# Optimization experiments

Hardware: AMD Instinct MI355X
Metric: run time of the kernel (lower is better)

Reference implementation:

```python
import jax, jax.numpy as jnp
import numpy as np

N = 1_000_000
VOCAB = 50_000
EMBED_DIM = 128
ENCODE_DIM = 128


def _random_preorder_tree(n, seed=0):
    """Generate a random tree whose nodes are numbered in pre-order DFS.
    Returns subtree_end[i] = index of the last node in node i's subtree (inclusive)."""
    rng = np.random.default_rng(seed)
    parent = np.empty(n, dtype=np.int64)
    parent[0] = -1
    stack = [0]
    pops = rng.geometric(0.5, size=n) - 1  # how far up to climb before attaching
    for i in range(1, n):
        npop = min(int(pops[i]), len(stack) - 1)
        for _ in range(npop):
            stack.pop()
        parent[i] = stack[-1]
        stack.append(i)
    end = np.arange(n, dtype=np.int64)
    for i in range(n - 1, 0, -1):
        p = parent[i]
        if end[p] < end[i]:
            end[p] = end[i]
    return end


def setup_inputs() -> dict:
    key = jax.random.key(0)
    k1, k2, k3, k4 = jax.random.split(key, 4)
    tokens = jax.random.randint(k1, (N,), 0, VOCAB, dtype=jnp.int64).astype(jnp.int32)
    subtree_end = jnp.asarray(_random_preorder_tree(N), dtype=jnp.int32)
    embedding_weight = jax.random.normal(k2, (VOCAB, EMBED_DIM), dtype=jnp.float32)
    W = jax.random.normal(k3, (ENCODE_DIM, EMBED_DIM), dtype=jnp.float32) * (1.0 / np.sqrt(EMBED_DIM))
    b = jax.random.normal(k4, (ENCODE_DIM,), dtype=jnp.float32) * 0.01
    return {"tokens": tokens, "subtree_end": subtree_end,
            "embedding_weight": embedding_weight, "W": W, "b": b}


def reference(tokens, subtree_end, embedding_weight, W, b):
    # Per-node contribution: x_i = Linear(Embed(token_i))          [N, encode_dim]
    x = embedding_weight[tokens] @ W.T + b
    # h_i = sum of x over subtree(i). With pre-order DFS numbering, the subtree
    # of i is the contiguous range [i, subtree_end[i]], so use an inclusive
    # prefix sum: h_i = S[end_i] - S[i] + x_i.
    S = jnp.cumsum(x, axis=0)                                      # [N, encode_dim]
    h = S[subtree_end] - S + x                                     # [N, encode_dim]
    # pool = max over all node hidden states (order-independent)
    return jnp.max(h, axis=0)                                      # [encode_dim]
```

## Files before the change

### kernel.cpp

```cpp
#include <hip/hip_runtime.h>
#include <hip/hip_bf16.h>

#define D      128
#define LG     9
#define CHUNK  512

typedef __attribute__((ext_vector_type(8))) short          short8;
typedef __attribute__((ext_vector_type(8))) unsigned short ushort8;
typedef __attribute__((ext_vector_type(4))) float          floatx4;
typedef __attribute__((ext_vector_type(2))) float          floatx2;

__device__ inline float b2f(unsigned short u) {
    return __uint_as_float(((unsigned)u) << 16);
}
__device__ inline unsigned short f2bf(float f) {
    __hip_bfloat16 h = __float2bfloat16(f);
    unsigned short u;
    __builtin_memcpy(&u, &h, 2);
    return u;
}
__device__ inline short8 u2s(ushort8 u) {
    short8 s; __builtin_memcpy(&s, &u, 16); return s;
}
__device__ inline void atomicMaxF(float* addr, float v) {
    if (v >= 0.f) atomicMax((int*)addr, __float_as_int(v));
    else          atomicMin((unsigned int*)addr, __float_as_uint(v));
}

__global__ void init_out_kernel(float* out, int out_size) {
    int t = threadIdx.x;
    if (t < out_size) out[t] = -INFINITY;
}

__global__ __launch_bounds__(256) void chunk_sums_kernel(
        const int* __restrict__ tokens, const float* __restrict__ emb,
        float* __restrict__ sumE, int n, int C) {
    __shared__ int toks[4][CHUNK];
    int tid = threadIdx.x, w = tid >> 6, lane = tid & 63;
    int cb = min(blockIdx.x * 4 + w, C - 1);
    int i0 = cb << LG, cnt = min(CHUNK, n - i0);
    for (int t = lane; t < cnt; t += 64) toks[w][t] = tokens[i0 + t];
    __syncthreads();
    const floatx2* eb = (const floatx2*)emb;
    float rx = 0.f, ry = 0.f;
    #pragma unroll 4
    for (int j = 0; j < cnt; ++j) {
        floatx2 v = eb[(size_t)toks[w][j] * 64 + lane];
        rx += v[0]; ry += v[1];
    }
    floatx2 rr = {rx, ry};
    *(floatx2*)(sumE + (size_t)cb * D + lane * 2) = rr;
}

__global__ void scan_kernel(float* sumE, int C) {
    int d    = blockIdx.x;
    int lane = threadIdx.x;
    float carry = 0.f;
    for (int c0 = 0; c0 < C; c0 += 64) {
        int c = c0 + lane;
        float v = (c < C) ? sumE[(size_t)c * D + d] : 0.f;
        float incl = v;
        #pragma unroll
        for (int off = 1; off < 64; off <<= 1) {
            float t = __shfl_up(incl, off);
            if (lane >= off) incl += t;
        }
        if (c < C) sumE[(size_t)c * D + d] = carry + incl - v;
        carry += __shfl(incl, 63);
    }
}

__global__ __launch_bounds__(128) void write_S_kernel(
        const int* __restrict__ tokens, const float* __restrict__ emb,
        const float* __restrict__ pref, unsigned* __restrict__ T32,
        int n, int C) {
    __shared__ int toks[2][CHUNK];
    int tid = threadIdx.x, w = tid >> 6, lane = tid & 63;
    int cb = min(blockIdx.x * 2 + w, C - 1);
    int i0 = cb << LG, cnt = min(CHUNK, n - i0);
    for (int t = lane; t < cnt; t += 64) toks[w][t] = tokens[i0 + t];
    __syncthreads();
    const floatx2* eb = (const floatx2*)emb;
    floatx2 r0 = *(const floatx2*)(pref + (size_t)cb * D + lane * 2);
    float rx = r0[0], ry = r0[1];
    unsigned* To = T32 + (size_t)i0 * 64 + lane;
    #pragma unroll 4
    for (int j = 0; j < cnt; ++j) {
        floatx2 v = eb[(size_t)toks[w][j] * 64 + lane];
        rx += v[0]; ry += v[1];
        unsigned pk = ((unsigned)f2bf(rx)) | (((unsigned)f2bf(ry)) << 16);
        __builtin_nontemporal_store(pk, To + (size_t)j * 64);
    }
}

__global__ __launch_bounds__(256, 2) void max_pass_kernel(
        const int* __restrict__ ends, const unsigned short* __restrict__ S,
        const float* __restrict__ W, const float* __restrict__ bvec,
        float* __restrict__ out, int n, int tpw) {
    __shared__ float red[4][8][16];
    int tid = threadIdx.x, lane = tid & 63, wid = tid >> 6;
    int c  = lane & 15;
    int kg = lane >> 4;

    short8 Wf[8][4];
    float  bc[8];
    #pragma unroll
    for (int tl = 0; tl < 8; ++tl) {
        const float* wr = W + (size_t)(tl * 16 + c) * D + kg * 8;
        bc[tl] = bvec[tl * 16 + c];
        #pragma unroll
        for (int kk = 0; kk < 4; ++kk) {
            floatx4 f0 = *(const floatx4*)(wr + kk * 32);
            floatx4 f1 = *(const floatx4*)(wr + kk * 32 + 4);
            short8 w;
            #pragma unroll
            for (int j = 0; j < 4; ++j) { w[j] = (short)f2bf(f0[j]); w[j + 4] = (short)f2bf(f1[j]); }
            Wf[tl][kk] = w;
        }
    }
    float mx[8];
    #pragma unroll
    for (int tl = 0; tl < 8; ++tl) mx[tl] = -INFINITY;

    const ushort8* Sv = (const ushort8*)S;
    int gw = blockIdx.x * 4 + wid;
    int STRIDE = gridDim.x * 4;
    ushort8 zero8 = {0, 0, 0, 0, 0, 0, 0, 0};

#define TIDX(k)  (gw + (k) * STRIDE)
#define LD_E(k)  ends[min(TIDX(k) * 16 + c, n - 1)]
#define LOAD_ROWS(k, e, Pe, Pp) do {                                     \
        int node_ = TIDX(k) * 16 + c;                                    \
        int pc_ = max(min(node_, n) - 1, 0);                             \
        const ushort8* pe_ = Sv + (size_t)(e) * 16 + kg;                 \
        const ushort8* pp_ = Sv + (size_t)pc_ * 16 + kg;                 \
        Pe[0] = pe_[0]; Pe[1] = pe_[4]; Pe[2] = pe_[8]; Pe[3] = pe_[12]; \
        Pp[0] = pp_[0]; Pp[1] = pp_[4]; Pp[2] = pp_[8]; Pp[3] = pp_[12]; \
        if (node_ == 0) { Pp[0] = zero8; Pp[1] = zero8; Pp[2] = zero8; Pp[3] = zero8; } \
    } while (0)

#define PROCESS(k, e, Pe, Pp) do {                                       \
        int base_ = TIDX(k) * 16;                                        \
        floatx4 cnt4_;                                                   \
        _Pragma("unroll")                                                \
        for (int i = 0; i < 4; ++i)                                      \
            cnt4_[i] = (float)(__shfl((e), kg * 4 + i) - (base_ + kg * 4 + i) + 1); \
        _Pragma("unroll")                                                \
        for (int tl = 0; tl < 8; ++tl) {                                 \
            floatx4 ae_ = {0.f, 0.f, 0.f, 0.f};                          \
            floatx4 ap_ = {0.f, 0.f, 0.f, 0.f};                          \
            _Pragma("unroll")                                            \
            for (int kk = 0; kk < 4; ++kk) {                             \
                ae_ = __builtin_amdgcn_mfma_f32_16x16x32_bf16(u2s(Pe[kk]), Wf[tl][kk], ae_, 0, 0, 0); \
                ap_ = __builtin_amdgcn_mfma_f32_16x16x32_bf16(u2s(Pp[kk]), Wf[tl][kk], ap_, 0, 0, 0); \
            }                                                            \
            _Pragma("unroll")                                            \
            for (int i = 0; i < 4; ++i) {                                \
                float h_ = (ae_[i] - ap_[i]) + cnt4_[i] * bc[tl];        \
                if (base_ + kg * 4 + i < n) mx[tl] = fmaxf(mx[tl], h_);  \
            }                                                            \
        }                                                                \
    } while (0)

    ushort8 Ae[4], Ap[4], Be[4], Bp[4];
    int e0 = LD_E(0);
    LOAD_ROWS(0, e0, Ae, Ap);
    int e1 = LD_E(1);
    for (int k = 0; k < tpw; k += 2) {
        LOAD_ROWS(k + 1, e1, Be, Bp);
        int e2 = LD_E(k + 2);
        PROCESS(k, e0, Ae, Ap);
        LOAD_ROWS(k + 2, e2, Ae, Ap);
        int e3 = LD_E(k + 3);
        PROCESS(k + 1, e1, Be, Bp);
        e0 = e2; e1 = e3;
    }

    #pragma unroll
    for (int tl = 0; tl < 8; ++tl) {
        float v = mx[tl];
        v = fmaxf(v, __shfl_xor(v, 16));
        v = fmaxf(v, __shfl_xor(v, 32));
        mx[tl] = v;
    }
    if (kg == 0) {
        #pragma unroll
        for (int tl = 0; tl < 8; ++tl) red[wid][tl][c] = mx[tl];
    }
    __syncthreads();
    if (tid < 128) {
        int tl = tid >> 4, cc = tid & 15;
        float v = fmaxf(fmaxf(red[0][tl][cc], red[1][tl][cc]),
                        fmaxf(red[2][tl][cc], red[3][tl][cc]));
        atomicMaxF(&out[tl * 16 + cc], v);
    }
}

extern "C" void kernel_launch(void* const* d_in, const int* in_sizes, int n_in,
                              void* d_out, int out_size, void* d_ws, size_t ws_size,
                              hipStream_t stream) {
    const int*   tokens = (const int*)d_in[0];
    const int*   ends   = (const int*)d_in[1];
    const float* emb    = (const float*)d_in[2];
    const float* W      = (const float*)d_in[3];
    const float* bvec   = (const float*)d_in[4];
    float* out = (float*)d_out;
    int n = in_sizes[0];
    int C = (n + CHUNK - 1) >> LG;

    unsigned short* S    = (unsigned short*)d_ws;
    float*          sumE = (float*)(S + (size_t)n * D);

    init_out_kernel<<<1, 128, 0, stream>>>(out, out_size);
    chunk_sums_kernel<<<(C + 3) / 4, 256, 0, stream>>>(tokens, emb, sumE, n, C);
    scan_kernel<<<128, 64, 0, stream>>>(sumE, C);
    write_S_kernel<<<(C + 1) / 2, 128, 0, stream>>>(tokens, emb, sumE,
                                                    (unsigned*)S, n, C);

    int n_tiles = (n + 15) / 16;
    int nblocks = 512;
    int waves   = nblocks * 4;
    int tpw = ((n_tiles + waves - 1) / waves + 1) & ~1;
    max_pass_kernel<<<nblocks, 256, 0, stream>>>(ends, S, W, bvec, out, n, tpw);
}
```

Baseline: 272.2 us.

## Store chunk-local prefix sums and add projected chunk offsets in max pass

The separate chunk-sum and write passes over the embedding gather are merged into one local scan that writes chunk-local bf16 prefix sums and chunk totals in a single pass. After the scan, a new small kernel projects the exclusive chunk prefixes through W. The max pass then adds the difference of the projected offsets for the end and start chunks. This removes one full gather pass over a million embedding rows. In exchange the max pass does extra scattered global loads, guarded by a branch, and the bf16 values now hold only local sums, which changes the rounding behaviour.

```diff
diff --git a/kernel.cpp b/kernel.cpp
--- a/kernel.cpp
+++ b/kernel.cpp
@@ -32,21 +32,24 @@
     if (t < out_size) out[t] = -INFINITY;
 }
 
-__global__ __launch_bounds__(256) void chunk_sums_kernel(
+__global__ __launch_bounds__(128) void local_scan_kernel(
         const int* __restrict__ tokens, const float* __restrict__ emb,
-        float* __restrict__ sumE, int n, int C) {
-    __shared__ int toks[4][CHUNK];
+        unsigned* __restrict__ T32, float* __restrict__ sumE, int n, int C) {
+    __shared__ int toks[2][CHUNK];
     int tid = threadIdx.x, w = tid >> 6, lane = tid & 63;
-    int cb = min(blockIdx.x * 4 + w, C - 1);
+    int cb = min(blockIdx.x * 2 + w, C - 1);
     int i0 = cb << LG, cnt = min(CHUNK, n - i0);
     for (int t = lane; t < cnt; t += 64) toks[w][t] = tokens[i0 + t];
     __syncthreads();
     const floatx2* eb = (const floatx2*)emb;
     float rx = 0.f, ry = 0.f;
+    unsigned* To = T32 + (size_t)i0 * 64 + lane;
     #pragma unroll 4
     for (int j = 0; j < cnt; ++j) {
         floatx2 v = eb[(size_t)toks[w][j] * 64 + lane];
         rx += v[0]; ry += v[1];
+        unsigned pk = ((unsigned)f2bf(rx)) | (((unsigned)f2bf(ry)) << 16);
+        __builtin_nontemporal_store(pk, To + (size_t)j * 64);
     }
     floatx2 rr = {rx, ry};
     *(floatx2*)(sumE + (size_t)cb * D + lane * 2) = rr;
@@ -70,33 +73,32 @@
     }
 }
 
-__global__ __launch_bounds__(128) void write_S_kernel(
-        const int* __restrict__ tokens, const float* __restrict__ emb,
-        const float* __restrict__ pref, unsigned* __restrict__ T32,
-        int n, int C) {
-    __shared__ int toks[2][CHUNK];
-    int tid = threadIdx.x, w = tid >> 6, lane = tid & 63;
-    int cb = min(blockIdx.x * 2 + w, C - 1);
-    int i0 = cb << LG, cnt = min(CHUNK, n - i0);
-    for (int t = lane; t < cnt; t += 64) toks[w][t] = tokens[i0 + t];
-    __syncthreads();
-    const floatx2* eb = (const floatx2*)emb;
-    floatx2 r0 = *(const floatx2*)(pref + (size_t)cb * D + lane * 2);
-    float rx = r0[0], ry = r0[1];
-    unsigned* To = T32 + (size_t)i0 * 64 + lane;
-    #pragma unroll 4
-    for (int j = 0; j < cnt; ++j) {
-        floatx2 v = eb[(size_t)toks[w][j] * 64 + lane];
-        rx += v[0]; ry += v[1];
-        unsigned pk = ((unsigned)f2bf(rx)) | (((unsigned)f2bf(ry)) << 16);
-        __builtin_nontemporal_store(pk, To + (size_t)j * 64);
-    }
+__global__ __launch_bounds__(128) void wp_kernel(
+        const float* __restrict__ W, float* __restrict__ P, int C) {
+    __shared__ float pl[16][D];
+    int d = threadIdx.x;
+    int c0 = blockIdx.x * 16;
+    int nr = min(16, C - c0);
+    for (int r = 0; r < nr; ++r) pl[r][d] = P[(size_t)(c0 + r) * D + d];
+    __syncthreads();
+    float acc[16];
+    #pragma unroll
+    for (int r = 0; r < 16; ++r) acc[r] = 0.f;
+    const float* wr = W + (size_t)d * D;
+    for (int k = 0; k < D; ++k) {
+        float wk = wr[k];
+        #pragma unroll
+        for (int r = 0; r < 16; ++r) acc[r] += wk * pl[r][k];
+    }
+    __syncthreads();
+    for (int r = 0; r < nr; ++r) P[(size_t)(c0 + r) * D + d] = acc[r];
 }
 
 __global__ __launch_bounds__(256, 2) void max_pass_kernel(
         const int* __restrict__ ends, const unsigned short* __restrict__ S,
-        const float* __restrict__ W, const float* __restrict__ bvec,
-        float* __restrict__ out, int n, int tpw) {
+        const float* __restrict__ WP, const float* __restrict__ W,
+        const float* __restrict__ bvec, float* __restrict__ out,
+        int n, int tpw, int Cm1) {
     __shared__ float red[4][8][16];
     int tid = threadIdx.x, lane = tid & 63, wid = tid >> 6;
     int c  = lane & 15;
@@ -142,9 +144,17 @@
 #define PROCESS(k, e, Pe, Pp) do {                                       \
         int base_ = TIDX(k) * 16;                                        \
         floatx4 cnt4_;                                                   \
+        int oe_[4], op_[4];                                              \
         _Pragma("unroll")                                                \
-        for (int i = 0; i < 4; ++i)                                      \
-            cnt4_[i] = (float)(__shfl((e), kg * 4 + i) - (base_ + kg * 4 + i) + 1); \
+        for (int i = 0; i < 4; ++i) {                                    \
+            int ei_ = __shfl((e), kg * 4 + i);                           \
+            int nd_ = base_ + kg * 4 + i;                                 \
+            cnt4_[i] = (float)(ei_ - nd_ + 1);                            \
+            int ce_ = min(ei_ >> LG, Cm1);                                \
+            int cp_ = min(max(nd_ - 1, 0) >> LG, Cm1);                    \
+            oe_[i] = (ce_ << 7) + c;                                      \
+            op_[i] = (cp_ << 7) + c;                                      \
+        }                                                                \
         _Pragma("unroll")                                                \
         for (int tl = 0; tl < 8; ++tl) {                                 \
             floatx4 ae_ = {0.f, 0.f, 0.f, 0.f};                          \
@@ -156,7 +166,10 @@
             }                                                            \
             _Pragma("unroll")                                            \
             for (int i = 0; i < 4; ++i) {                                \
-                float h_ = (ae_[i] - ap_[i]) + cnt4_[i] * bc[tl];        \
+                float corr_ = 0.f;                                       \
+                if (oe_[i] != op_[i])                                    \
+                    corr_ = WP[oe_[i] + tl * 16] - WP[op_[i] + tl * 16]; \
+                float h_ = (ae_[i] - ap_[i]) + corr_ + cnt4_[i] * bc[tl];\
                 if (base_ + kg * 4 + i < n) mx[tl] = fmaxf(mx[tl], h_);  \
             }                                                            \
         }                                                                \
@@ -212,14 +225,15 @@
     float*          sumE = (float*)(S + (size_t)n * D);
 
     init_out_kernel<<<1, 128, 0, stream>>>(out, out_size);
-    chunk_sums_kernel<<<(C + 3) / 4, 256, 0, stream>>>(tokens, emb, sumE, n, C);
+    local_scan_kernel<<<(C + 1) / 2, 128, 0, stream>>>(tokens, emb,
+                                                       (unsigned*)S, sumE, n, C);
     scan_kernel<<<128, 64, 0, stream>>>(sumE, C);
-    write_S_kernel<<<(C + 1) / 2, 128, 0, stream>>>(tokens, emb, sumE,
-                                                    (unsigned*)S, n, C);
+    wp_kernel<<<(C + 15) / 16, 128, 0, stream>>>(W, sumE, C);
 
     int n_tiles = (n + 15) / 16;
     int nblocks = 512;
     int waves   = nblocks * 4;
     int tpw = ((n_tiles + waves - 1) / waves + 1) & ~1;
-    max_pass_kernel<<<nblocks, 256, 0, stream>>>(ends, S, W, bvec, out, n, tpw);
-}
+    max_pass_kernel<<<nblocks, 256, 0, stream>>>(ends, S, sumE, W, bvec, out,
+                                                 n, tpw, C - 1);
+}
```

Result: slower. 369.2 us (+35.6%).

## Store chunk-local prefix sums and add chunk offsets via extra MFMA in max pass

Applied to the files above, without the earlier changes.

The S array is written during the first gather pass as chunk-local prefix sums, which removes the second full embedding-gather pass (write_S_kernel). The scan kernel also emits a bf16 copy of the per-chunk exclusive offsets. The max pass adds those offsets through extra MFMAs on the offset rows. To keep register pressure in check, waves are paired and each handles half of the output columns. This doubles the MFMA work and adds offset-row loads in the max pass, and it splits rows across two waves, so every S row is loaded twice.

```diff
diff --git a/kernel.cpp b/kernel.cpp
--- a/kernel.cpp
+++ b/kernel.cpp
@@ -32,27 +32,30 @@
     if (t < out_size) out[t] = -INFINITY;
 }
 
-__global__ __launch_bounds__(256) void chunk_sums_kernel(
+__global__ __launch_bounds__(128) void local_scan_kernel(
         const int* __restrict__ tokens, const float* __restrict__ emb,
-        float* __restrict__ sumE, int n, int C) {
-    __shared__ int toks[4][CHUNK];
+        unsigned* __restrict__ T32, float* __restrict__ sumE, int n, int C) {
+    __shared__ int toks[2][CHUNK];
     int tid = threadIdx.x, w = tid >> 6, lane = tid & 63;
-    int cb = min(blockIdx.x * 4 + w, C - 1);
+    int cb = min(blockIdx.x * 2 + w, C - 1);
     int i0 = cb << LG, cnt = min(CHUNK, n - i0);
     for (int t = lane; t < cnt; t += 64) toks[w][t] = tokens[i0 + t];
     __syncthreads();
     const floatx2* eb = (const floatx2*)emb;
     float rx = 0.f, ry = 0.f;
+    unsigned* To = T32 + (size_t)i0 * 64 + lane;
     #pragma unroll 4
     for (int j = 0; j < cnt; ++j) {
         floatx2 v = eb[(size_t)toks[w][j] * 64 + lane];
         rx += v[0]; ry += v[1];
+        unsigned pk = ((unsigned)f2bf(rx)) | (((unsigned)f2bf(ry)) << 16);
+        __builtin_nontemporal_store(pk, To + (size_t)j * 64);
     }
     floatx2 rr = {rx, ry};
     *(floatx2*)(sumE + (size_t)cb * D + lane * 2) = rr;
 }
 
-__global__ void scan_kernel(float* sumE, int C) {
+__global__ void scan_kernel(float* sumE, unsigned short* prefB, int C) {
     int d    = blockIdx.x;
     int lane = threadIdx.x;
     float carry = 0.f;
@@ -65,49 +68,33 @@
             float t = __shfl_up(incl, off);
             if (lane >= off) incl += t;
         }
-        if (c < C) sumE[(size_t)c * D + d] = carry + incl - v;
+        if (c < C) {
+            float exc = carry + incl - v;
+            sumE[(size_t)c * D + d] = exc;
+            prefB[(size_t)c * D + d] = f2bf(exc);
+        }
         carry += __shfl(incl, 63);
-    }
-}
-
-__global__ __launch_bounds__(128) void write_S_kernel(
-        const int* __restrict__ tokens, const float* __restrict__ emb,
-        const float* __restrict__ pref, unsigned* __restrict__ T32,
-        int n, int C) {
-    __shared__ int toks[2][CHUNK];
-    int tid = threadIdx.x, w = tid >> 6, lane = tid & 63;
-    int cb = min(blockIdx.x * 2 + w, C - 1);
-    int i0 = cb << LG, cnt = min(CHUNK, n - i0);
-    for (int t = lane; t < cnt; t += 64) toks[w][t] = tokens[i0 + t];
-    __syncthreads();
-    const floatx2* eb = (const floatx2*)emb;
-    floatx2 r0 = *(const floatx2*)(pref + (size_t)cb * D + lane * 2);
-    float rx = r0[0], ry = r0[1];
-    unsigned* To = T32 + (size_t)i0 * 64 + lane;
-    #pragma unroll 4
-    for (int j = 0; j < cnt; ++j) {
-        floatx2 v = eb[(size_t)toks[w][j] * 64 + lane];
-        rx += v[0]; ry += v[1];
-        unsigned pk = ((unsigned)f2bf(rx)) | (((unsigned)f2bf(ry)) << 16);
-        __builtin_nontemporal_store(pk, To + (size_t)j * 64);
     }
 }
 
 __global__ __launch_bounds__(256, 2) void max_pass_kernel(
         const int* __restrict__ ends, const unsigned short* __restrict__ S,
-        const float* __restrict__ W, const float* __restrict__ bvec,
-        float* __restrict__ out, int n, int tpw) {
-    __shared__ float red[4][8][16];
+        const unsigned short* __restrict__ prefB, const float* __restrict__ W,
+        const float* __restrict__ bvec, float* __restrict__ out,
+        int n, int tpw) {
+    __shared__ float red[4][4][16];
     int tid = threadIdx.x, lane = tid & 63, wid = tid >> 6;
     int c  = lane & 15;
     int kg = lane >> 4;
-
-    short8 Wf[8][4];
-    float  bc[8];
+    int tw = wid & 1;
+    int pr = wid >> 1;
+
+    short8 Wf[4][4];
+    float  bc[4];
     #pragma unroll
-    for (int tl = 0; tl < 8; ++tl) {
-        const float* wr = W + (size_t)(tl * 16 + c) * D + kg * 8;
-        bc[tl] = bvec[tl * 16 + c];
+    for (int tl = 0; tl < 4; ++tl) {
+        const float* wr = W + (size_t)((tw * 4 + tl) * 16 + c) * D + kg * 8;
+        bc[tl] = bvec[(tw * 4 + tl) * 16 + c];
         #pragma unroll
         for (int kk = 0; kk < 4; ++kk) {
             floatx4 f0 = *(const floatx4*)(wr + kk * 32);
@@ -118,41 +105,54 @@
             Wf[tl][kk] = w;
         }
     }
-    float mx[8];
+    float mx[4];
     #pragma unroll
-    for (int tl = 0; tl < 8; ++tl) mx[tl] = -INFINITY;
+    for (int tl = 0; tl < 4; ++tl) mx[tl] = -INFINITY;
 
     const ushort8* Sv = (const ushort8*)S;
-    int gw = blockIdx.x * 4 + wid;
-    int STRIDE = gridDim.x * 4;
+    const ushort8* PB = (const ushort8*)prefB;
+    int gp = blockIdx.x * 2 + pr;
+    int STRIDE = gridDim.x * 2;
     ushort8 zero8 = {0, 0, 0, 0, 0, 0, 0, 0};
 
-#define TIDX(k)  (gw + (k) * STRIDE)
+#define TIDX(k)  (gp + (k) * STRIDE)
 #define LD_E(k)  ends[min(TIDX(k) * 16 + c, n - 1)]
-#define LOAD_ROWS(k, e, Pe, Pp) do {                                     \
-        int node_ = TIDX(k) * 16 + c;                                    \
+#define LOAD_EROWS(k, e, QE, SE) do {                                    \
+        int ce_ = (e) >> LG;                                             \
+        const ushort8* se_ = Sv + (size_t)(e) * 16 + kg;                 \
+        const ushort8* qe_ = PB + (size_t)ce_ * 16 + kg;                 \
+        SE[0] = se_[0]; SE[1] = se_[4]; SE[2] = se_[8]; SE[3] = se_[12]; \
+        QE[0] = qe_[0]; QE[1] = qe_[4]; QE[2] = qe_[8]; QE[3] = qe_[12]; \
+    } while (0)
+
+#define PROCESS(k, e, QE, SE) do {                                       \
+        int base_ = TIDX(k) * 16;                                        \
+        int node_ = base_ + c;                                           \
         int pc_ = max(min(node_, n) - 1, 0);                             \
-        const ushort8* pe_ = Sv + (size_t)(e) * 16 + kg;                 \
-        const ushort8* pp_ = Sv + (size_t)pc_ * 16 + kg;                 \
-        Pe[0] = pe_[0]; Pe[1] = pe_[4]; Pe[2] = pe_[8]; Pe[3] = pe_[12]; \
-        Pp[0] = pp_[0]; Pp[1] = pp_[4]; Pp[2] = pp_[8]; Pp[3] = pp_[12]; \
-        if (node_ == 0) { Pp[0] = zero8; Pp[1] = zero8; Pp[2] = zero8; Pp[3] = zero8; } \
-    } while (0)
-
-#define PROCESS(k, e, Pe, Pp) do {                                       \
-        int base_ = TIDX(k) * 16;                                        \
+        int cp_ = pc_ >> LG;                                             \
+        const ushort8* sp_ = Sv + (size_t)pc_ * 16 + kg;                 \
+        const ushort8* qp_ = PB + (size_t)cp_ * 16 + kg;                 \
+        ushort8 SP[4], QP[4];                                            \
+        SP[0] = sp_[0]; SP[1] = sp_[4]; SP[2] = sp_[8]; SP[3] = sp_[12]; \
+        QP[0] = qp_[0]; QP[1] = qp_[4]; QP[2] = qp_[8]; QP[3] = qp_[12]; \
+        if (node_ == 0) { SP[0] = zero8; SP[1] = zero8; SP[2] = zero8; SP[3] = zero8; } \
         floatx4 cnt4_;                                                   \
         _Pragma("unroll")                                                \
         for (int i = 0; i < 4; ++i)                                      \
             cnt4_[i] = (float)(__shfl((e), kg * 4 + i) - (base_ + kg * 4 + i) + 1); \
         _Pragma("unroll")                                                \
-        for (int tl = 0; tl < 8; ++tl) {                                 \
+        for (int tl = 0; tl < 4; ++tl) {                                 \
             floatx4 ae_ = {0.f, 0.f, 0.f, 0.f};                          \
             floatx4 ap_ = {0.f, 0.f, 0.f, 0.f};                          \
             _Pragma("unroll")                                            \
             for (int kk = 0; kk < 4; ++kk) {                             \
-                ae_ = __builtin_amdgcn_mfma_f32_16x16x32_bf16(u2s(Pe[kk]), Wf[tl][kk], ae_, 0, 0, 0); \
-                ap_ = __builtin_amdgcn_mfma_f32_16x16x32_bf16(u2s(Pp[kk]), Wf[tl][kk], ap_, 0, 0, 0); \
+                ae_ = __builtin_amdgcn_mfma_f32_16x16x32_bf16(u2s(QE[kk]), Wf[tl][kk], ae_, 0, 0, 0); \
+                ap_ = __builtin_amdgcn_mfma_f32_16x16x32_bf16(u2s(QP[kk]), Wf[tl][kk], ap_, 0, 0, 0); \
+            }                                                            \
+            _Pragma("unroll")                                            \
+            for (int kk = 0; kk < 4; ++kk) {                             \
+                ae_ = __builtin_amdgcn_mfma_f32_16x16x32_bf16(u2s(SE[kk]), Wf[tl][kk], ae_, 0, 0, 0); \
+                ap_ = __builtin_amdgcn_mfma_f32_16x16x32_bf16(u2s(SP[kk]), Wf[tl][kk], ap_, 0, 0, 0); \
             }                                                            \
             _Pragma("unroll")                                            \
             for (int i = 0; i < 4; ++i) {                                \
@@ -162,22 +162,22 @@
         }                                                                \
     } while (0)
 
-    ushort8 Ae[4], Ap[4], Be[4], Bp[4];
+    ushort8 QEa[4], SEa[4], QEb[4], SEb[4];
     int e0 = LD_E(0);
-    LOAD_ROWS(0, e0, Ae, Ap);
+    LOAD_EROWS(0, e0, QEa, SEa);
     int e1 = LD_E(1);
     for (int k = 0; k < tpw; k += 2) {
-        LOAD_ROWS(k + 1, e1, Be, Bp);
+        LOAD_EROWS(k + 1, e1, QEb, SEb);
         int e2 = LD_E(k + 2);
-        PROCESS(k, e0, Ae, Ap);
-        LOAD_ROWS(k + 2, e2, Ae, Ap);
+        PROCESS(k, e0, QEa, SEa);
+        LOAD_EROWS(k + 2, e2, QEa, SEa);
         int e3 = LD_E(k + 3);
-        PROCESS(k + 1, e1, Be, Bp);
+        PROCESS(k + 1, e1, QEb, SEb);
         e0 = e2; e1 = e3;
     }
 
     #pragma unroll
-    for (int tl = 0; tl < 8; ++tl) {
+    for (int tl = 0; tl < 4; ++tl) {
         float v = mx[tl];
         v = fmaxf(v, __shfl_xor(v, 16));
         v = fmaxf(v, __shfl_xor(v, 32));
@@ -185,14 +185,15 @@
     }
     if (kg == 0) {
         #pragma unroll
-        for (int tl = 0; tl < 8; ++tl) red[wid][tl][c] = mx[tl];
+        for (int tl = 0; tl < 4; ++tl) red[wid][tl][c] = mx[tl];
     }
     __syncthreads();
     if (tid < 128) {
-        int tl = tid >> 4, cc = tid & 15;
-        float v = fmaxf(fmaxf(red[0][tl][cc], red[1][tl][cc]),
-                        fmaxf(red[2][tl][cc], red[3][tl][cc]));
-        atomicMaxF(&out[tl * 16 + cc], v);
+        int twf = tid >> 6;
+        int tl  = (tid >> 4) & 3;
+        int cc  = tid & 15;
+        float v = fmaxf(red[twf][tl][cc], red[twf + 2][tl][cc]);
+        atomicMaxF(&out[(twf * 4 + tl) * 16 + cc], v);
     }
 }
 
@@ -208,18 +209,19 @@
     int n = in_sizes[0];
     int C = (n + CHUNK - 1) >> LG;
 
-    unsigned short* S    = (unsigned short*)d_ws;
-    float*          sumE = (float*)(S + (size_t)n * D);
+    unsigned short* S     = (unsigned short*)d_ws;
+    float*          sumE  = (float*)(S + (size_t)n * D);
+    unsigned short* prefB = (unsigned short*)(sumE + (size_t)C * D);
 
     init_out_kernel<<<1, 128, 0, stream>>>(out, out_size);
-    chunk_sums_kernel<<<(C + 3) / 4, 256, 0, stream>>>(tokens, emb, sumE, n, C);
-    scan_kernel<<<128, 64, 0, stream>>>(sumE, C);
-    write_S_kernel<<<(C + 1) / 2, 128, 0, stream>>>(tokens, emb, sumE,
-                                                    (unsigned*)S, n, C);
+    local_scan_kernel<<<(C + 1) / 2, 128, 0, stream>>>(tokens, emb,
+                                                       (unsigned*)S, sumE, n, C);
+    scan_kernel<<<128, 64, 0, stream>>>(sumE, prefB, C);
 
     int n_tiles = (n + 15) / 16;
     int nblocks = 512;
-    int waves   = nblocks * 4;
-    int tpw = ((n_tiles + waves - 1) / waves + 1) & ~1;
-    max_pass_kernel<<<nblocks, 256, 0, stream>>>(ends, S, W, bvec, out, n, tpw);
-}
+    int pairs   = nblocks * 2;
+    int tpw = ((n_tiles + pairs - 1) / pairs + 1) & ~1;
+    max_pass_kernel<<<nblocks, 256, 0, stream>>>(ends, S, prefB, W, bvec, out,
+                                                 n, tpw);
+}
```

Result: no change. 273.0 us (+0.3%).
